# Performance work log

Hardware: AMD Instinct MI355X
Metric: run time of the kernel (lower is better)

## Reference

```python
import jax, jax.numpy as jnp
import numpy as np
from jax import lax


def _conv(x, w, b, pad, groups):
    # NCHW conv, kernel OIHW, stride 1, symmetric padding, grouped.
    y = lax.conv_general_dilated(
        x, w, window_strides=(1, 1), padding=[(pad, pad), (pad, pad)],
        dimension_numbers=("NCHW", "OIHW", "NCHW"), feature_group_count=groups)
    return y if b is None else y + b[None, :, None, None]


def setup_inputs() -> dict:
    key = jax.random.key(0)
    ks = jax.random.split(key, 8)
    B, C, H, W = 8, 128, 128, 128
    nh = 8
    c3 = C * 3            # pos conv output channels
    o = (C // 2) * 3      # each QKV dconv output channels (3C/2)
    ch = C // 2           # SSA dconv output channels
    s = 0.05
    return {
        "x": jax.random.normal(ks[0], (B, C, H, W), jnp.float32),
        "pos_w": jax.random.normal(ks[1], (c3, C, 1, 1), jnp.float32) * s,
        "pos_b": jnp.zeros((c3,), jnp.float32),
        "qd3_w": jax.random.normal(ks[2], (o, 2, 3, 3), jnp.float32) * s,
        "qd3_b": jnp.zeros((o,), jnp.float32),
        "qd5_w": jax.random.normal(ks[3], (o, 2, 5, 5), jnp.float32) * s,
        "qd5_b": jnp.zeros((o,), jnp.float32),
        "temp": jnp.ones((nh, 1, 1), jnp.float32),
        "d3_w": jax.random.normal(ks[4], (ch, 2, 3, 3), jnp.float32) * s,
        "d3_b": jnp.zeros((ch,), jnp.float32),
        "d5_w": jax.random.normal(ks[5], (ch, 2, 5, 5), jnp.float32) * s,
        "d5_b": jnp.zeros((ch,), jnp.float32),
        "proj_w": jax.random.normal(ks[6], (C, 2 * C, 1, 1), jnp.float32) * s,
        "num_head": 8,
    }


def _l2norm(a):
    # F.normalize(dim=-1): x / max(||x||, 1e-12)
    n = jnp.sqrt(jnp.sum(a * a, axis=-1, keepdims=True))
    return a / jnp.maximum(n, 1e-12)


def reference(x, pos_w, pos_b, qd3_w, qd3_b, qd5_w, qd5_b, temp,
              d3_w, d3_b, d5_w, d5_b, proj_w, num_head):
    B, C, H, W = x.shape
    hw = H * W
    # QKV module: 1x1 pos conv -> two grouped dconvs (groups = out channels = 3C/2) -> concat
    t = _conv(x, pos_w, pos_b, 0, 1)                      # (B, 3C, H, W)
    g = qd3_w.shape[0]                                     # 3C/2 groups
    qkv = jnp.concatenate(
        (_conv(t, qd3_w, qd3_b, 1, g), _conv(t, qd5_w, qd5_b, 2, g)), axis=1)  # (B, 3C, H, W)
    qkv = qkv.reshape(B, 3, num_head, -1, hw)              # (B, 3, nh, d, hw)
    q, k, v = qkv[:, 0], qkv[:, 1], qkv[:, 2]
    q = _l2norm(q)
    k = _l2norm(k)
    # transposed (channel) attention: d x d per head, temperature-scaled softmax
    attn = jax.nn.softmax(jnp.einsum("bhdn,bhen->bhde", q, k) * temp[None], axis=-1)
    out = jnp.einsum("bhde,bhen->bhdn", attn, v).reshape(B, C, H, W)
    ch = C // 2
    y = jnp.concatenate(
        (out, _conv(x, d3_w, d3_b, 1, ch), _conv(x, d5_w, d5_b, 2, ch)), axis=1)  # (B, 2C, H, W)
    return _conv(y, proj_w, None, 0, 1)                    # 1x1 proj, no bias
```

## Files before the change

### kernel.cpp

```cpp
#include <hip/hip_runtime.h>
#include <hip/hip_bf16.h>


#define HW 16384
#define HH 128
#define WW 128

typedef __attribute__((ext_vector_type(8))) short bf16x8;
typedef __attribute__((ext_vector_type(8))) _Float16 f16x8;
typedef __attribute__((ext_vector_type(4))) float f32x4;
typedef __attribute__((ext_vector_type(4))) unsigned short us4;
typedef __fp16 fp16x2 __attribute__((ext_vector_type(2)));

__device__ inline unsigned short f2bf(float f) {
    unsigned u = __float_as_uint(f);
    return (unsigned short)((u + 0x7FFFu + ((u >> 16) & 1u)) >> 16);
}
__device__ inline unsigned packbf(float lo, float hi) {
    return (unsigned)f2bf(lo) | ((unsigned)f2bf(hi) << 16);
}
__device__ inline unsigned short f2h(float f) {
    _Float16 h = (_Float16)f;
    return __builtin_bit_cast(unsigned short, h);
}
__device__ inline unsigned packh(float lo, float hi) {
    return (unsigned)f2h(lo) | ((unsigned)f2h(hi) << 16);
}
__device__ inline unsigned packh2(float lo, float hi) {
    fp16x2 h = __builtin_amdgcn_cvt_pkrtz(lo, hi);
    return __builtin_bit_cast(unsigned, h);
}

__device__ inline float dot2acc(unsigned a, unsigned b, float c) {
    float d;
    asm("v_dot2_f32_f16 %0, %1, %2, %3" : "=v"(d) : "v"(a), "v"(b), "v"(c));
    return d;
}

__global__ void zerok(float* p, int n) {
    int i = blockIdx.x * 256 + threadIdx.x;
    if (i < n) p[i] = 0.f;
}

__global__ __launch_bounds__(256) void packw(const float* __restrict__ w,
                                             unsigned* __restrict__ wpk) {
    int id = blockIdx.x * 256 + threadIdx.x;
    if (id >= 384 * 64) return;
    int m = id >> 6, kp = id & 63;
    wpk[id] = packh(w[m * 128 + 2 * kp], w[m * 128 + 2 * kp + 1]);
}

__global__ __launch_bounds__(256) void packcw(
    const float* __restrict__ qd3, const float* __restrict__ qd5,
    const float* __restrict__ d3, const float* __restrict__ d5,
    unsigned* __restrict__ o) {
    int id = blockIdx.x * 256 + threadIdx.x;
    if (id < 192 * 9) {
        int g = id / 9, tp = id % 9;
        o[id] = packh(qd3[(g * 2) * 9 + tp], qd3[(g * 2 + 1) * 9 + tp]);
    } else if (id < 192 * 9 + 192 * 25) {
        int r = id - 192 * 9; int g = r / 25, tp = r % 25;
        o[id] = packh(qd5[(g * 2) * 25 + tp], qd5[(g * 2 + 1) * 25 + tp]);
    } else if (id < 192 * 9 + 192 * 25 + 64 * 9) {
        int r = id - 192 * 9 - 192 * 25; int g = r / 9, tp = r % 9;
        o[id] = packh(d3[(g * 2) * 9 + tp], d3[(g * 2 + 1) * 9 + tp]);
    } else if (id < 192 * 9 + 192 * 25 + 64 * 9 + 64 * 25) {
        int r = id - 192 * 9 - 192 * 25 - 64 * 9; int g = r / 25, tp = r % 25;
        o[id] = packh(d5[(g * 2) * 25 + tp], d5[(g * 2 + 1) * 25 + tp]);
    }
}

__global__ __launch_bounds__(256) void gemm_t(
    const unsigned* __restrict__ wpk,
    const float* __restrict__ x,
    const float* __restrict__ posb,
    unsigned* __restrict__ tpk)
{
    int b = blockIdx.z;
    int n0 = blockIdx.x * 64;
    const float* xb = x + (long)b * 128 * HW;
    unsigned* tb = tpk + (long)b * 192 * HW;
    __shared__ unsigned Bs[64][65];
    int tid = threadIdx.x;
    {
        int kp = tid >> 2, nq = tid & 3;
        const float* s0 = xb + (long)(2 * kp) * HW + n0 + nq * 16;
        const float* s1 = s0 + HW;
        int nb_ = nq * 16;
        #pragma unroll
        for (int q4 = 0; q4 < 4; ++q4) {
            float4 lo = *(const float4*)(s0 + q4 * 4);
            float4 hi = *(const float4*)(s1 + q4 * 4);
            Bs[nb_ + q4 * 4 + 0][kp] = packh2(lo.x, hi.x);
            Bs[nb_ + q4 * 4 + 1][kp] = packh2(lo.y, hi.y);
            Bs[nb_ + q4 * 4 + 2][kp] = packh2(lo.z, hi.z);
            Bs[nb_ + q4 * 4 + 3][kp] = packh2(lo.w, hi.w);
        }
    }
    __syncthreads();
    int w = tid >> 6, l = tid & 63;
    int lr = l & 15, lg = l >> 4;
    f32x4 acc[6][4] = {};
    #pragma unroll
    for (int kk = 0; kk < 4; ++kk) {
        f16x8 af[6];
        #pragma unroll
        for (int mt = 0; mt < 6; ++mt) {
            int m = (w * 6 + mt) * 16 + lr;
            af[mt] = *(const f16x8*)(wpk + (long)m * 64 + kk * 16 + lg * 4);
        }
        #pragma unroll
        for (int ns = 0; ns < 4; ++ns) {
            f16x8 bf = *(const f16x8*)(&Bs[ns * 16 + lr][kk * 16 + lg * 4]);
            #pragma unroll
            for (int mt = 0; mt < 6; ++mt)
                acc[mt][ns] = __builtin_amdgcn_mfma_f32_16x16x32_f16(
                    af[mt], bf, acc[mt][ns], 0, 0, 0);
        }
    }
    #pragma unroll
    for (int mt = 0; mt < 6; ++mt) {
        int m0 = w * 96 + mt * 16 + lg * 4;
        float b0v = posb[m0], b1v = posb[m0 + 1], b2v = posb[m0 + 2], b3v = posb[m0 + 3];
        int p0 = m0 >> 1;
        #pragma unroll
        for (int ns = 0; ns < 4; ++ns) {
            int col = n0 + ns * 16 + lr;
            tb[(long)p0 * HW + col]       = packh2(acc[mt][ns][0] + b0v, acc[mt][ns][1] + b1v);
            tb[(long)(p0 + 1) * HW + col] = packh2(acc[mt][ns][2] + b2v, acc[mt][ns][3] + b3v);
        }
    }
}

template<bool PK>
__global__ __launch_bounds__(256) void dualconv(
    const void* __restrict__ src_, int srcCP,
    const unsigned* __restrict__ w3pk, const float* __restrict__ b3,
    const unsigned* __restrict__ w5pk, const float* __restrict__ b5,
    int s3, unsigned short* __restrict__ r3a, long st3a,
    unsigned short* __restrict__ r3b, long st3b,
    int s5, unsigned short* __restrict__ r5a, long st5a,
    unsigned short* __restrict__ r5b, long st5b)
{
    int gp = blockIdx.y, b = blockIdx.z, y0 = blockIdx.x * 8;
    __shared__ __align__(16) unsigned tile[2][12][132];
    int tid = threadIdx.x;
    const unsigned* sU = (const unsigned*)src_ + ((long)b * srcCP + 2 * gp) * HW;
    const float*    sF = (const float*)src_ + ((long)b * srcCP + 4 * gp) * HW;
    const int TOT = 2 * 12 * 132;
    for (int idx = tid; idx < TOT; idx += 256) {
        int gi = idx / (12 * 132);
        int rem = idx - gi * (12 * 132);
        int r = rem / 132, ci = rem - r * 132;
        int row = y0 + r - 2, col = ci - 2;
        unsigned u = 0;
        if ((unsigned)row < (unsigned)HH && (unsigned)col < (unsigned)WW) {
            long o = (long)row * WW + col;
            u = PK ? sU[(long)gi * HW + o]
                   : packh2(sF[(long)(2 * gi) * HW + o], sF[(long)(2 * gi + 1) * HW + o]);
        }
        tile[gi][r][ci] = u;
    }
    __syncthreads();
    int xq = tid & 31, yy = tid >> 5;
    int x0 = xq * 4;
    float a3[2][4], a5[2][4];
    #pragma unroll
    for (int gi = 0; gi < 2; ++gi) {
        int g = 2 * gp + gi;
        #pragma unroll
        for (int j = 0; j < 4; ++j) { a3[gi][j] = b3[g]; a5[gi][j] = b5[g]; }
        unsigned w5v[25], w3v[9];
        #pragma unroll
        for (int i = 0; i < 25; ++i) w5v[i] = w5pk[g * 25 + i];
        #pragma unroll
        for (int i = 0; i < 9; ++i) w3v[i] = w3pk[g * 9 + i];
        #pragma unroll
        for (int r = 0; r < 5; ++r) {
            const unsigned* p = &tile[gi][yy + r][x0];
            unsigned win[8];
            *(f32x4*)win = *(const f32x4*)p;
            *(f32x4*)(win + 4) = *(const f32x4*)(p + 4);
            #pragma unroll
            for (int dx = 0; dx < 5; ++dx)
                #pragma unroll
                for (int j = 0; j < 4; ++j)
                    a5[gi][j] = dot2acc(win[j + dx], w5v[r * 5 + dx], a5[gi][j]);
            if (r >= 1 && r <= 3) {
                #pragma unroll
                for (int dx = 0; dx < 3; ++dx)
                    #pragma unroll
                    for (int j = 0; j < 4; ++j)
                        a3[gi][j] = dot2acc(win[j + dx + 1], w3v[(r - 1) * 3 + dx], a3[gi][j]);
            }
        }
    }
    long prow = (long)(y0 + yy) * WW + x0;
    #pragma unroll
    for (int gi = 0; gi < 2; ++gi) {
        int g = 2 * gp + gi;
        uint2 v3, v5;
        v3.x = packbf(a3[gi][0], a3[gi][1]);
        v3.y = packbf(a3[gi][2], a3[gi][3]);
        v5.x = packbf(a5[gi][0], a5[gi][1]);
        v5.y = packbf(a5[gi][2], a5[gi][3]);
        unsigned short* d3 = (g < s3) ? r3a + (long)b * st3a + (long)g * HW
                                      : r3b + (long)b * st3b + (long)(g - s3) * HW;
        unsigned short* d5 = (g < s5) ? r5a + (long)b * st5a + (long)g * HW
                                      : r5b + (long)b * st5b + (long)(g - s5) * HW;
        *(uint2*)(d3 + prow) = v3;
        *(uint2*)(d5 + prow) = v5;
    }
}

__global__ __launch_bounds__(64) void gram_mfma(
    const unsigned short* __restrict__ q,
    const unsigned short* __restrict__ k,
    float* __restrict__ gbuf)
{
    int bh = blockIdx.x, chunk = blockIdx.y;
    int b = bh >> 3, h = bh & 7;
    int l = threadIdx.x;
    int r = l & 15, koff = (l >> 4) * 8;
    const unsigned short* qrow = q + ((long)b * 128 + h * 16 + r) * HW;
    const unsigned short* krow = k + ((long)b * 128 + h * 16 + r) * HW;
    f32x4 accS = {0.f, 0.f, 0.f, 0.f};
    f32x4 accQ = {0.f, 0.f, 0.f, 0.f};
    f32x4 accK = {0.f, 0.f, 0.f, 0.f};
    int n0 = chunk * 512;
    for (int n = n0; n < n0 + 512; n += 32) {
        bf16x8 af = *(const bf16x8*)(qrow + n + koff);
        bf16x8 bf = *(const bf16x8*)(krow + n + koff);
        accS = __builtin_amdgcn_mfma_f32_16x16x32_bf16(af, bf, accS, 0, 0, 0);
        accQ = __builtin_amdgcn_mfma_f32_16x16x32_bf16(af, af, accQ, 0, 0, 0);
        accK = __builtin_amdgcn_mfma_f32_16x16x32_bf16(bf, bf, accK, 0, 0, 0);
    }
    float* gb = gbuf + bh * 288;
    #pragma unroll
    for (int reg = 0; reg < 4; ++reg) {
        int row = (l >> 4) * 4 + reg;
        atomicAdd(&gb[row * 16 + r], accS[reg]);
        if (row == r) {
            atomicAdd(&gb[256 + r], accQ[reg]);
            atomicAdd(&gb[272 + r], accK[reg]);
        }
    }
}

__global__ __launch_bounds__(256) void attn_fold(
    const float* __restrict__ gbuf, const float* __restrict__ temp,
    const float* __restrict__ projw,
    unsigned* __restrict__ wallpk)
{
    int bh = blockIdx.x;
    int b = bh >> 3, h = bh & 7;
    const float* gb = gbuf + bh * 288;
    __shared__ float logit[16][16];
    __shared__ float A[16][16];
    int tid = threadIdx.x;
    int d = tid >> 4, e = tid & 15;
    {
        float nq = fmaxf(sqrtf(gb[256 + d]), 1e-12f);
        float nk = fmaxf(sqrtf(gb[272 + e]), 1e-12f);
        logit[d][e] = gb[d * 16 + e] / (nq * nk) * temp[h];
    }
    __syncthreads();
    float m = -1e30f;
    #pragma unroll
    for (int j = 0; j < 16; ++j) m = fmaxf(m, logit[d][j]);
    float ex = expf(logit[d][e] - m);
    A[d][e] = ex;
    __syncthreads();
    float sum = 0.f;
    #pragma unroll
    for (int j = 0; j < 16; ++j) sum += A[d][j];
    __syncthreads();
    A[d][e] = ex / sum;
    __syncthreads();
    int ep = tid & 7, co0 = tid >> 3;
    for (int co = co0; co < 128; co += 32) {
        float lo = 0.f, hi = 0.f;
        #pragma unroll
        for (int dd = 0; dd < 16; ++dd) {
            float pw = projw[co * 256 + h * 16 + dd];
            lo += pw * A[dd][2 * ep];
            hi += pw * A[dd][2 * ep + 1];
        }
        wallpk[((long)b * 128 + co) * 128 + h * 8 + ep] = packbf(lo, hi);
    }
    if (h == 0) {
        for (int idx = tid; idx < 128 * 64; idx += 256) {
            int co = idx >> 6, cp = idx & 63;
            wallpk[((long)b * 128 + co) * 128 + 64 + cp] =
                packbf(projw[co * 256 + 128 + 2 * cp], projw[co * 256 + 129 + 2 * cp]);
        }
    }
}

__global__ __launch_bounds__(256) void gemm_out(
    const unsigned* __restrict__ wpk,
    const unsigned short* __restrict__ vy,
    float* __restrict__ out)
{
    int b = blockIdx.z;
    int n0 = blockIdx.x * 64;
    const unsigned* wb = wpk + (long)b * 128 * 128;
    const unsigned short* vyb = vy + (long)b * 256 * HW;
    float* ob = out + (long)b * 128 * HW;
    __shared__ unsigned Bs[64][129];
    int tid = threadIdx.x;
    {
        int kp = tid >> 1, nh = (tid & 1) * 32;
        const unsigned short* s0 = vyb + (long)(2 * kp) * HW + n0 + nh;
        const unsigned short* s1 = s0 + HW;
        #pragma unroll
        for (int q4 = 0; q4 < 4; ++q4) {
            us4 lo0 = *(const us4*)(s0 + q4 * 8);
            us4 lo1 = *(const us4*)(s0 + q4 * 8 + 4);
            us4 hi0 = *(const us4*)(s1 + q4 * 8);
            us4 hi1 = *(const us4*)(s1 + q4 * 8 + 4);
            #pragma unroll
            for (int j = 0; j < 4; ++j) {
                Bs[nh + q4 * 8 + j][kp]     = (unsigned)lo0[j] | ((unsigned)hi0[j] << 16);
                Bs[nh + q4 * 8 + 4 + j][kp] = (unsigned)lo1[j] | ((unsigned)hi1[j] << 16);
            }
        }
    }
    __syncthreads();
    int w = tid >> 6, l = tid & 63;
    int lr = l & 15, lg = l >> 4;
    f32x4 acc[2][4] = {};
    #pragma unroll
    for (int kk = 0; kk < 8; ++kk) {
        bf16x8 af[2];
        #pragma unroll
        for (int i = 0; i < 2; ++i) {
            int m = (w * 2 + i) * 16 + lr;
            af[i] = *(const bf16x8*)(wb + (long)m * 128 + kk * 16 + lg * 4);
        }
        #pragma unroll
        for (int ns = 0; ns < 4; ++ns) {
            bf16x8 bf = *(const bf16x8*)(&Bs[ns * 16 + lr][kk * 16 + lg * 4]);
            #pragma unroll
            for (int i = 0; i < 2; ++i)
                acc[i][ns] = __builtin_amdgcn_mfma_f32_16x16x32_bf16(
                    af[i], bf, acc[i][ns], 0, 0, 0);
        }
    }
    #pragma unroll
    for (int i = 0; i < 2; ++i)
        #pragma unroll
        for (int ns = 0; ns < 4; ++ns)
            #pragma unroll
            for (int reg = 0; reg < 4; ++reg) {
                int m = (w * 2 + i) * 16 + lg * 4 + reg;
                ob[(long)m * HW + n0 + ns * 16 + lr] = acc[i][ns][reg];
            }
}

extern "C" void kernel_launch(void* const* d_in, const int* in_sizes, int n_in,
                              void* d_out, int out_size, void* d_ws, size_t ws_size,
                              hipStream_t stream) {
    const float* x      = (const float*)d_in[0];
    const float* pos_w  = (const float*)d_in[1];
    const float* pos_b  = (const float*)d_in[2];
    const float* qd3_w  = (const float*)d_in[3];
    const float* qd3_b  = (const float*)d_in[4];
    const float* qd5_w  = (const float*)d_in[5];
    const float* qd5_b  = (const float*)d_in[6];
    const float* temp   = (const float*)d_in[7];
    const float* d3_w   = (const float*)d_in[8];
    const float* d3_b   = (const float*)d_in[9];
    const float* d5_w   = (const float*)d_in[10];
    const float* d5_b   = (const float*)d_in[11];
    const float* proj_w = (const float*)d_in[12];
    float* out = (float*)d_out;

    size_t perb = (size_t)HW * 1792 + 65536;
    size_t fixedb = 64UL * 288 * 4 + 384UL * 64 * 4 + 8704UL * 4;
    int NB = 8;
    while (NB > 1 && (size_t)NB * perb + fixedb > ws_size) NB >>= 1;

    char* base = (char*)d_ws;
    unsigned* tpk      = (unsigned*)base;       base += (size_t)NB * 192 * HW * 4;
    unsigned short* qb = (unsigned short*)base; base += (size_t)NB * 128 * HW * 2;
    unsigned short* kb = (unsigned short*)base; base += (size_t)NB * 128 * HW * 2;
    unsigned short* vy = (unsigned short*)base; base += (size_t)NB * 256 * HW * 2;
    unsigned* wallpk   = (unsigned*)base;       base += (size_t)NB * 128 * 128 * 4;
    float* gram        = (float*)base;          base += 64UL * 288 * 4;
    unsigned* poswpk   = (unsigned*)base;       base += 384UL * 64 * 4;
    unsigned* cwpk     = (unsigned*)base;
    unsigned* qd3pk = cwpk;
    unsigned* qd5pk = cwpk + 192 * 9;
    unsigned* d3pk  = cwpk + 192 * 9 + 192 * 25;
    unsigned* d5pk  = cwpk + 192 * 9 + 192 * 25 + 64 * 9;

    packw<<<(384 * 64 + 255) / 256, 256, 0, stream>>>(pos_w, poswpk);
    packcw<<<(8704 + 255) / 256, 256, 0, stream>>>(qd3_w, qd5_w, d3_w, d5_w, cwpk);

    for (int b0 = 0; b0 < 8; b0 += NB) {
        const float* xb = x + (long)b0 * 128 * HW;
        float* outb = out + (long)b0 * 128 * HW;

        gemm_t<<<dim3(HW / 64, 1, NB), 256, 0, stream>>>(poswpk, xb, pos_b, tpk);

        dualconv<false><<<dim3(16, 32, NB), 256, 0, stream>>>(
            xb, 128, d3pk, d3_b, d5pk, d5_b,
            64, vy + 128L * HW, 256L * HW, vy + 128L * HW, 256L * HW,
            64, vy + 192L * HW, 256L * HW, vy + 192L * HW, 256L * HW);

        dualconv<true><<<dim3(16, 96, NB), 256, 0, stream>>>(
            tpk, 192, qd3pk, qd3_b, qd5pk, qd5_b,
            128, qb, 128L * HW, kb, 128L * HW,
            64, kb + 64L * HW, 128L * HW, vy, 256L * HW);

        zerok<<<(64 * 288 + 255) / 256, 256, 0, stream>>>(gram, 64 * 288);
        gram_mfma<<<dim3(NB * 8, 32), 64, 0, stream>>>(qb, kb, gram);
        attn_fold<<<NB * 8, 256, 0, stream>>>(gram, temp, proj_w, wallpk);

        gemm_out<<<dim3(HW / 64, 1, NB), 256, 0, stream>>>(wallpk, vy, outb);
    }
}
```

Measured before the change: 240.5 us.

## Emit packed fp16 x from pos GEMM and enlarge dualconv tiles to 16 rows

The pos-conv GEMM now also writes a packed fp16 pair copy of x into workspace (aliased onto the q buffer region). The SSA dualconv reads that copy instead of converting fp32 x again. dualconv now processes 16 output rows per block with 8 outputs per thread, which lowers halo overhead and widens stores. The cost is higher register pressure, an extra global write in the GEMM, and xpk aliasing qb/kb space, which is safe only because the SSA dualconv runs before the q/k dualconv overwrites it.

```diff
diff --git a/kernel.cpp b/kernel.cpp
--- a/kernel.cpp
+++ b/kernel.cpp
@@ -74,7 +74,8 @@
     const unsigned* __restrict__ wpk,
     const float* __restrict__ x,
     const float* __restrict__ posb,
-    unsigned* __restrict__ tpk)
+    unsigned* __restrict__ tpk,
+    unsigned* __restrict__ xpk)
 {
     int b = blockIdx.z;
     int n0 = blockIdx.x * 64;
@@ -86,15 +87,22 @@
         int kp = tid >> 2, nq = tid & 3;
         const float* s0 = xb + (long)(2 * kp) * HW + n0 + nq * 16;
         const float* s1 = s0 + HW;
+        unsigned* xo = xpk + (long)b * 64 * HW + (long)kp * HW + n0 + nq * 16;
         int nb_ = nq * 16;
         #pragma unroll
         for (int q4 = 0; q4 < 4; ++q4) {
             float4 lo = *(const float4*)(s0 + q4 * 4);
             float4 hi = *(const float4*)(s1 + q4 * 4);
-            Bs[nb_ + q4 * 4 + 0][kp] = packh2(lo.x, hi.x);
-            Bs[nb_ + q4 * 4 + 1][kp] = packh2(lo.y, hi.y);
-            Bs[nb_ + q4 * 4 + 2][kp] = packh2(lo.z, hi.z);
-            Bs[nb_ + q4 * 4 + 3][kp] = packh2(lo.w, hi.w);
+            uint4 o;
+            o.x = packh2(lo.x, hi.x);
+            o.y = packh2(lo.y, hi.y);
+            o.z = packh2(lo.z, hi.z);
+            o.w = packh2(lo.w, hi.w);
+            Bs[nb_ + q4 * 4 + 0][kp] = o.x;
+            Bs[nb_ + q4 * 4 + 1][kp] = o.y;
+            Bs[nb_ + q4 * 4 + 2][kp] = o.z;
+            Bs[nb_ + q4 * 4 + 3][kp] = o.w;
+            *(uint4*)(xo + q4 * 4) = o;
         }
     }
     __syncthreads();
@@ -132,9 +140,8 @@
     }
 }
 
-template<bool PK>
 __global__ __launch_bounds__(256) void dualconv(
-    const void* __restrict__ src_, int srcCP,
+    const unsigned* __restrict__ src, int srcP,
     const unsigned* __restrict__ w3pk, const float* __restrict__ b3,
     const unsigned* __restrict__ w5pk, const float* __restrict__ b5,
     int s3, unsigned short* __restrict__ r3a, long st3a,
@@ -142,34 +149,30 @@
     int s5, unsigned short* __restrict__ r5a, long st5a,
     unsigned short* __restrict__ r5b, long st5b)
 {
-    int gp = blockIdx.y, b = blockIdx.z, y0 = blockIdx.x * 8;
-    __shared__ __align__(16) unsigned tile[2][12][132];
+    int gp = blockIdx.y, b = blockIdx.z, y0 = blockIdx.x * 16;
+    __shared__ __align__(16) unsigned tile[2][20][132];
     int tid = threadIdx.x;
-    const unsigned* sU = (const unsigned*)src_ + ((long)b * srcCP + 2 * gp) * HW;
-    const float*    sF = (const float*)src_ + ((long)b * srcCP + 4 * gp) * HW;
-    const int TOT = 2 * 12 * 132;
+    const unsigned* sU = src + ((long)b * srcP + 2 * gp) * HW;
+    const int TOT = 2 * 20 * 132;
     for (int idx = tid; idx < TOT; idx += 256) {
-        int gi = idx / (12 * 132);
-        int rem = idx - gi * (12 * 132);
+        int gi = idx / (20 * 132);
+        int rem = idx - gi * (20 * 132);
         int r = rem / 132, ci = rem - r * 132;
         int row = y0 + r - 2, col = ci - 2;
         unsigned u = 0;
-        if ((unsigned)row < (unsigned)HH && (unsigned)col < (unsigned)WW) {
-            long o = (long)row * WW + col;
-            u = PK ? sU[(long)gi * HW + o]
-                   : packh2(sF[(long)(2 * gi) * HW + o], sF[(long)(2 * gi + 1) * HW + o]);
-        }
+        if ((unsigned)row < (unsigned)HH && (unsigned)col < (unsigned)WW)
+            u = sU[(long)gi * HW + row * WW + col];
         tile[gi][r][ci] = u;
     }
     __syncthreads();
-    int xq = tid & 31, yy = tid >> 5;
-    int x0 = xq * 4;
-    float a3[2][4], a5[2][4];
+    int xq = tid & 15, yy = tid >> 4;
+    int x0 = xq * 8;
+    float a3[2][8], a5[2][8];
     #pragma unroll
     for (int gi = 0; gi < 2; ++gi) {
         int g = 2 * gp + gi;
         #pragma unroll
-        for (int j = 0; j < 4; ++j) { a3[gi][j] = b3[g]; a5[gi][j] = b5[g]; }
+        for (int j = 0; j < 8; ++j) { a3[gi][j] = b3[g]; a5[gi][j] = b5[g]; }
         unsigned w5v[25], w3v[9];
         #pragma unroll
         for (int i = 0; i < 25; ++i) w5v[i] = w5pk[g * 25 + i];
@@ -178,19 +181,20 @@
         #pragma unroll
         for (int r = 0; r < 5; ++r) {
             const unsigned* p = &tile[gi][yy + r][x0];
-            unsigned win[8];
+            unsigned win[12];
             *(f32x4*)win = *(const f32x4*)p;
             *(f32x4*)(win + 4) = *(const f32x4*)(p + 4);
+            *(f32x4*)(win + 8) = *(const f32x4*)(p + 8);
             #pragma unroll
             for (int dx = 0; dx < 5; ++dx)
                 #pragma unroll
-                for (int j = 0; j < 4; ++j)
+                for (int j = 0; j < 8; ++j)
                     a5[gi][j] = dot2acc(win[j + dx], w5v[r * 5 + dx], a5[gi][j]);
             if (r >= 1 && r <= 3) {
                 #pragma unroll
                 for (int dx = 0; dx < 3; ++dx)
                     #pragma unroll
-                    for (int j = 0; j < 4; ++j)
+                    for (int j = 0; j < 8; ++j)
                         a3[gi][j] = dot2acc(win[j + dx + 1], w3v[(r - 1) * 3 + dx], a3[gi][j]);
             }
         }
@@ -199,17 +203,21 @@
     #pragma unroll
     for (int gi = 0; gi < 2; ++gi) {
         int g = 2 * gp + gi;
-        uint2 v3, v5;
+        uint4 v3, v5;
         v3.x = packbf(a3[gi][0], a3[gi][1]);
         v3.y = packbf(a3[gi][2], a3[gi][3]);
+        v3.z = packbf(a3[gi][4], a3[gi][5]);
+        v3.w = packbf(a3[gi][6], a3[gi][7]);
         v5.x = packbf(a5[gi][0], a5[gi][1]);
         v5.y = packbf(a5[gi][2], a5[gi][3]);
+        v5.z = packbf(a5[gi][4], a5[gi][5]);
+        v5.w = packbf(a5[gi][6], a5[gi][7]);
         unsigned short* d3 = (g < s3) ? r3a + (long)b * st3a + (long)g * HW
                                       : r3b + (long)b * st3b + (long)(g - s3) * HW;
         unsigned short* d5 = (g < s5) ? r5a + (long)b * st5a + (long)g * HW
                                       : r5b + (long)b * st5b + (long)(g - s5) * HW;
-        *(uint2*)(d3 + prow) = v3;
-        *(uint2*)(d5 + prow) = v5;
+        *(uint4*)(d3 + prow) = v3;
+        *(uint4*)(d5 + prow) = v5;
     }
 }
 
@@ -383,6 +391,7 @@
 
     char* base = (char*)d_ws;
     unsigned* tpk      = (unsigned*)base;       base += (size_t)NB * 192 * HW * 4;
+    unsigned* xpk      = (unsigned*)base;
     unsigned short* qb = (unsigned short*)base; base += (size_t)NB * 128 * HW * 2;
     unsigned short* kb = (unsigned short*)base; base += (size_t)NB * 128 * HW * 2;
     unsigned short* vy = (unsigned short*)base; base += (size_t)NB * 256 * HW * 2;
@@ -402,14 +411,14 @@
         const float* xb = x + (long)b0 * 128 * HW;
         float* outb = out + (long)b0 * 128 * HW;
 
-        gemm_t<<<dim3(HW / 64, 1, NB), 256, 0, stream>>>(poswpk, xb, pos_b, tpk);
-
-        dualconv<false><<<dim3(16, 32, NB), 256, 0, stream>>>(
-            xb, 128, d3pk, d3_b, d5pk, d5_b,
+        gemm_t<<<dim3(HW / 64, 1, NB), 256, 0, stream>>>(poswpk, xb, pos_b, tpk, xpk);
+
+        dualconv<<<dim3(8, 32, NB), 256, 0, stream>>>(
+            xpk, 64, d3pk, d3_b, d5pk, d5_b,
             64, vy + 128L * HW, 256L * HW, vy + 128L * HW, 256L * HW,
             64, vy + 192L * HW, 256L * HW, vy + 192L * HW, 256L * HW);
 
-        dualconv<true><<<dim3(16, 96, NB), 256, 0, stream>>>(
+        dualconv<<<dim3(8, 96, NB), 256, 0, stream>>>(
             tpk, 192, qd3pk, qd3_b, qd5pk, qd5_b,
             128, qb, 128L * HW, kb, 128L * HW,
             64, kb + 64L * HW, 128L * HW, vy, 256L * HW);
```

New measurement: 223.1 us. -7.2%, faster.
